# Kernel tuning notes

Measured on AMD Instinct MI355X. Metric: run time of the kernel, lower is better.

Reference implementation:

```python
import jax, jax.numpy as jnp
import numpy as np

K = 50
EPS = 1e-8


def setup_inputs() -> dict:
    key = jax.random.key(0)
    k1, k2 = jax.random.split(key)
    B, S, V = 2, 2048, 50257
    p = jax.random.uniform(k1, (B, S, V), dtype=jnp.float32)
    q = jax.random.uniform(k2, (B, S, V), dtype=jnp.float32)
    # normalize to probability distributions over the vocab dim
    p = p / jnp.sum(p, axis=-1, keepdims=True)
    q = q / jnp.sum(q, axis=-1, keepdims=True)
    return {"p": p, "q": q}


def _kl(p, q):
    p_safe = p + EPS
    q_safe = q + EPS
    return jnp.sum(p_safe * jnp.log(p_safe / q_safe), axis=-1)


def reference(p, q):
    B, S, V = p.shape
    N = B * S
    p_flat = p.reshape(N, V)
    q_flat = q.reshape(N, V)

    _, p_idx = jax.lax.top_k(p_flat, K)  # [N, K]
    _, q_idx = jax.lax.top_k(q_flat, K)  # [N, K]

    rows = jnp.arange(N)[:, None]  # [N, 1]
    mask = jnp.zeros((N, V), dtype=bool)
    mask = mask.at[rows, p_idx].set(True)
    mask = mask.at[rows, q_idx].set(True)

    p_m = jnp.where(mask, p_flat, 0.0)
    q_m = jnp.where(mask, q_flat, 0.0)

    p_m = p_m / (jnp.sum(p_m, axis=-1, keepdims=True) + EPS)
    q_m = q_m / (jnp.sum(q_m, axis=-1, keepdims=True) + EPS)

    m = 0.5 * (p_m + q_m)
    jsd = 0.5 * _kl(p_m, m) + 0.5 * _kl(q_m, m)  # [N]
    return jsd.reshape(B, S)
```

## Files before the change

### kernel.cpp

```cpp
#include <hip/hip_runtime.h>
#include <stdint.h>

#define NTHREADS 256
#define KTOP 50
#define CAP 1024
#define CAPREF 512
#define EPSV 1e-8f

typedef unsigned long long u64;

#define C_CNTP 0
#define C_CNTQ 1
#define C_REFP 2
#define C_REFQ 3

__device__ __forceinline__ float block_max(float v, float* s_f, int tid) {
    for (int off = 32; off; off >>= 1) v = fmaxf(v, __shfl_down(v, off));
    if ((tid & 63) == 0) s_f[tid >> 6] = v;
    __syncthreads();
    if (tid == 0) {
        float m = s_f[0];
        for (int w = 1; w < NTHREADS / 64; ++w) m = fmaxf(m, s_f[w]);
        s_f[4] = m;
    }
    __syncthreads();
    float r = s_f[4];
    __syncthreads();
    return r;
}

__device__ __forceinline__ void push_cand(u64* cand, uint32_t* cnt,
                                          float v, int idx, float t) {
    if (v >= t) {
        uint32_t pos = atomicAdd(cnt, 1u);
        if (pos < CAP)
            cand[pos] = (((u64)__float_as_uint(v)) << 16) |
                        (u64)(0xFFFFu - (uint32_t)idx);
    }
}

__device__ int collect_direct(const float* __restrict__ row, int V, float t,
                              u64* cand, uint32_t* s_cnt, int tid) {
    if (tid == 0) *s_cnt = 0;
    __syncthreads();
    int mis = (int)(((uintptr_t)row >> 2) & 3);
    int head = (4 - mis) & 3; if (head > V) head = V;
    if (tid < head) push_cand(cand, s_cnt, row[tid], tid, t);
    int nvec = (V - head) >> 2;
    const float4* vr = reinterpret_cast<const float4*>(row + head);
    for (int i = tid; i < nvec; i += NTHREADS) {
        float4 v = vr[i];
        int b = head + (i << 2);
        push_cand(cand, s_cnt, v.x, b, t);     push_cand(cand, s_cnt, v.y, b + 1, t);
        push_cand(cand, s_cnt, v.z, b + 2, t); push_cand(cand, s_cnt, v.w, b + 3, t);
    }
    for (int i = head + (nvec << 2) + tid; i < V; i += NTHREADS)
        push_cand(cand, s_cnt, row[i], i, t);
    __syncthreads();
    int n = (int)*s_cnt;
    __syncthreads();
    return n;
}

__device__ __forceinline__ float max16(float4 a, float4 b, float4 c, float4 d) {
    float m0 = fmaxf(fmaxf(a.x, a.y), fmaxf(a.z, a.w));
    float m1 = fmaxf(fmaxf(b.x, b.y), fmaxf(b.z, b.w));
    float m2 = fmaxf(fmaxf(c.x, c.y), fmaxf(c.z, c.w));
    float m3 = fmaxf(fmaxf(d.x, d.y), fmaxf(d.z, d.w));
    return fmaxf(fmaxf(m0, m1), fmaxf(m2, m3));
}

__device__ void find_topk(const u64* cand, int nc, uint16_t* top,
                          u64* s_merge, int tid) {
    int lane = tid & 63, w = tid >> 6;
    u64 r0 = 0, r1 = 0, r2 = 0, r3 = 0;
    int j0 = (w << 6) + lane;
    if (j0 < nc)       r0 = cand[j0];
    if (j0 + 256 < nc) r1 = cand[j0 + 256];
    if (j0 + 512 < nc) r2 = cand[j0 + 512];
    if (j0 + 768 < nc) r3 = cand[j0 + 768];
    for (int k = 0; k < KTOP; ++k) {
        u64 a = r0 > r1 ? r0 : r1;
        u64 b = r2 > r3 ? r2 : r3;
        u64 m = a > b ? a : b;
        #pragma unroll
        for (int off = 32; off; off >>= 1) {
            u64 o = __shfl_xor(m, off);
            if (o > m) m = o;
        }
        if (lane == 0) s_merge[w * KTOP + k] = m;
        if (r0 == m) r0 = 0; else if (r1 == m) r1 = 0;
        else if (r2 == m) r2 = 0; else if (r3 == m) r3 = 0;
    }
    __syncthreads();
    if (w == 0) {
        u64 q0 = 0, q1 = 0, q2 = 0, q3 = 0;
        if (lane < 4 * KTOP)       q0 = s_merge[lane];
        if (lane + 64 < 4 * KTOP)  q1 = s_merge[lane + 64];
        if (lane + 128 < 4 * KTOP) q2 = s_merge[lane + 128];
        if (lane + 192 < 4 * KTOP) q3 = s_merge[lane + 192];
        for (int k = 0; k < KTOP; ++k) {
            u64 a = q0 > q1 ? q0 : q1;
            u64 b = q2 > q3 ? q2 : q3;
            u64 m = a > b ? a : b;
            #pragma unroll
            for (int off = 32; off; off >>= 1) {
                u64 o = __shfl_xor(m, off);
                if (o > m) m = o;
            }
            if (lane == 0) top[k] = (uint16_t)(0xFFFFu - (uint32_t)(m & 0xFFFFu));
            if (q0 == m) q0 = 0; else if (q1 == m) q1 = 0;
            else if (q2 == m) q2 = 0; else if (q3 == m) q3 = 0;
        }
    }
    __syncthreads();
}

__global__ __launch_bounds__(NTHREADS, 4)
void topk_jsd_kernel(const float* __restrict__ p, const float* __restrict__ q,
                     float* __restrict__ out, int V)
{
    __shared__ u64 candP[CAP];
    __shared__ u64 candQ[CAP];
    __shared__ uint32_t refsP[CAPREF];
    __shared__ uint32_t refsQ[CAPREF];
    __shared__ u64 s_merge[4 * KTOP];
    __shared__ float s_f[8];
    __shared__ uint32_t s_c[4];
    __shared__ uint16_t topP[KTOP];
    __shared__ uint16_t topQ[KTOP];
    __shared__ uint16_t s_union[2 * KTOP];
    __shared__ int s_nu;

    const int row = blockIdx.x;
    const int tid = threadIdx.x;
    const float* prow = p + (size_t)row * (size_t)V;
    const float* qrow = q + (size_t)row * (size_t)V;

    int smp = V < 2048 ? V : 2048;
    float msP = 0.f, msQ = 0.f;
    for (int i = tid; i < smp; i += NTHREADS) {
        msP = fmaxf(msP, prow[i]);
        msQ = fmaxf(msQ, qrow[i]);
    }
    float MsP = block_max(msP, s_f, tid);
    float MsQ = block_max(msQ, s_f, tid);

    float eps0 = fminf(128.f / (float)V + 1.f / (float)smp, 0.5f);
    float tP = MsP * (1.f - eps0);
    float tQ = MsQ * (1.f - eps0);

    int misP = (int)(((uintptr_t)prow >> 2) & 3);
    int misQ = (int)(((uintptr_t)qrow >> 2) & 3);
    int headP = (4 - misP) & 3; if (headP > V) headP = V;
    int headQ = (4 - misQ) & 3; if (headQ > V) headQ = V;

    int ncP = -1, ncQ = -1;
    if (headP == headQ) {
        int head = headP;
        if (tid == 0) { s_c[0] = 0; s_c[1] = 0; s_c[2] = 0; s_c[3] = 0; }
        __syncthreads();
        int nvec = (V - head) >> 2;
        const float4* vp = reinterpret_cast<const float4*>(prow + head);
        const float4* vq = reinterpret_cast<const float4*>(qrow + head);
        const int per = 4 * NTHREADS;
        int ngrp = nvec / per;

        if (tid < head) {
            push_cand(candP, &s_c[C_CNTP], prow[tid], tid, tP);
            push_cand(candQ, &s_c[C_CNTQ], qrow[tid], tid, tQ);
        }
        #pragma unroll 2
        for (int g = 0; g < ngrp; ++g) {
            int o = g * per + tid;
            float4 a0 = vp[o];
            float4 a1 = vp[o + NTHREADS];
            float4 a2 = vp[o + 2 * NTHREADS];
            float4 a3 = vp[o + 3 * NTHREADS];
            float4 b0 = vq[o];
            float4 b1 = vq[o + NTHREADS];
            float4 b2 = vq[o + 2 * NTHREADS];
            float4 b3 = vq[o + 3 * NTHREADS];
            float mp = max16(a0, a1, a2, a3);
            float mq = max16(b0, b1, b2, b3);
            if (mp >= tP) {
                uint32_t rp = atomicAdd(&s_c[C_REFP], 1u);
                if (rp < CAPREF) refsP[rp] = (uint32_t)o;
            }
            if (mq >= tQ) {
                uint32_t rq = atomicAdd(&s_c[C_REFQ], 1u);
                if (rq < CAPREF) refsQ[rq] = (uint32_t)o;
            }
        }
        for (int i = ngrp * per + tid; i < nvec; i += NTHREADS) {
            float4 a = vp[i], b = vq[i];
            int e = head + (i << 2);
            push_cand(candP, &s_c[C_CNTP], a.x, e, tP);     push_cand(candP, &s_c[C_CNTP], a.y, e + 1, tP);
            push_cand(candP, &s_c[C_CNTP], a.z, e + 2, tP); push_cand(candP, &s_c[C_CNTP], a.w, e + 3, tP);
            push_cand(candQ, &s_c[C_CNTQ], b.x, e, tQ);     push_cand(candQ, &s_c[C_CNTQ], b.y, e + 1, tQ);
            push_cand(candQ, &s_c[C_CNTQ], b.z, e + 2, tQ); push_cand(candQ, &s_c[C_CNTQ], b.w, e + 3, tQ);
        }
        for (int i = head + (nvec << 2) + tid; i < V; i += NTHREADS) {
            push_cand(candP, &s_c[C_CNTP], prow[i], i, tP);
            push_cand(candQ, &s_c[C_CNTQ], qrow[i], i, tQ);
        }
        __syncthreads();
        uint32_t nrefP = s_c[C_REFP], nrefQ = s_c[C_REFQ];
        if (nrefP <= CAPREF) {
            int units = (int)nrefP * 4;
            for (int u = tid; u < units; u += NTHREADS) {
                int f4 = (int)refsP[u >> 2] + (u & 3) * NTHREADS;
                float4 v = vp[f4];
                int e = head + (f4 << 2);
                push_cand(candP, &s_c[C_CNTP], v.x, e, tP);     push_cand(candP, &s_c[C_CNTP], v.y, e + 1, tP);
                push_cand(candP, &s_c[C_CNTP], v.z, e + 2, tP); push_cand(candP, &s_c[C_CNTP], v.w, e + 3, tP);
            }
        }
        if (nrefQ <= CAPREF) {
            int units = (int)nrefQ * 4;
            for (int u = tid; u < units; u += NTHREADS) {
                int f4 = (int)refsQ[u >> 2] + (u & 3) * NTHREADS;
                float4 v = vq[f4];
                int e = head + (f4 << 2);
                push_cand(candQ, &s_c[C_CNTQ], v.x, e, tQ);     push_cand(candQ, &s_c[C_CNTQ], v.y, e + 1, tQ);
                push_cand(candQ, &s_c[C_CNTQ], v.z, e + 2, tQ); push_cand(candQ, &s_c[C_CNTQ], v.w, e + 3, tQ);
            }
        }
        __syncthreads();
        ncP = (nrefP <= CAPREF) ? (int)s_c[C_CNTP] : -1;
        ncQ = (nrefQ <= CAPREF) ? (int)s_c[C_CNTQ] : -1;
        __syncthreads();
    }

    {
        float eps = eps0;
        if (ncP < 0) ncP = collect_direct(prow, V, MsP * (1.f - eps), candP, &s_c[C_CNTP], tid);
        for (int a = 0; a < 10 && (ncP < KTOP || ncP > CAP); ++a) {
            eps = (ncP > CAP) ? eps * 0.25f : fminf(eps * 4.f, 1.f);
            ncP = collect_direct(prow, V, MsP * (1.f - eps), candP, &s_c[C_CNTP], tid);
        }
        if (ncP > CAP) ncP = CAP;
    }
    {
        float eps = eps0;
        if (ncQ < 0) ncQ = collect_direct(qrow, V, MsQ * (1.f - eps), candQ, &s_c[C_CNTQ], tid);
        for (int a = 0; a < 10 && (ncQ < KTOP || ncQ > CAP); ++a) {
            eps = (ncQ > CAP) ? eps * 0.25f : fminf(eps * 4.f, 1.f);
            ncQ = collect_direct(qrow, V, MsQ * (1.f - eps), candQ, &s_c[C_CNTQ], tid);
        }
        if (ncQ > CAP) ncQ = CAP;
    }

    find_topk(candP, ncP, topP, s_merge, tid);
    find_topk(candQ, ncQ, topQ, s_merge, tid);

    if (tid < KTOP) s_union[tid] = topP[tid];
    __syncthreads();
    if (tid < 64) {
        bool fresh = false; uint16_t qi = 0;
        if (tid < KTOP) {
            qi = topQ[tid]; fresh = true;
            for (int j = 0; j < KTOP; ++j) if (topP[j] == qi) fresh = false;
        }
        unsigned long long mb = __ballot(fresh);
        int pos = __popcll(mb & ((1ull << tid) - 1ull));
        if (fresh) s_union[KTOP + pos] = qi;
        if (tid == 0) s_nu = KTOP + __popcll(mb);
    }
    __syncthreads();
    int nu = s_nu;

    float pv = 0.f, qv = 0.f;
    if (tid < nu) {
        int ui = s_union[tid];
        pv = prow[ui];
        qv = qrow[ui];
    }

    float sp = pv, sq = qv;
    for (int off = 32; off; off >>= 1) { sp += __shfl_down(sp, off); sq += __shfl_down(sq, off); }
    int wid = tid >> 6;
    if ((tid & 63) == 0) { s_f[wid] = sp; s_f[4 + wid] = sq; }
    __syncthreads();
    if (tid == 0) {
        float a = 0.f, b = 0.f;
        for (int w = 0; w < NTHREADS / 64; ++w) { a += s_f[w]; b += s_f[4 + w]; }
        s_f[0] = a; s_f[4] = b;
    }
    __syncthreads();
    float sump = s_f[0], sumq = s_f[4];
    __syncthreads();

    float term = 0.f;
    if (tid < nu) {
        float pn = pv / (sump + EPSV);
        float qn = qv / (sumq + EPSV);
        float mn = 0.5f * (pn + qn);
        float ps = pn + EPSV, qs = qn + EPSV, ms = mn + EPSV;
        term = 0.5f * (ps * logf(ps / ms) + qs * logf(qs / ms));
    }
    for (int off = 32; off; off >>= 1) term += __shfl_down(term, off);
    if ((tid & 63) == 0) s_f[wid] = term;
    __syncthreads();
    if (tid == 0) {
        float a = 0.f;
        for (int w = 0; w < NTHREADS / 64; ++w) a += s_f[w];
        out[row] = a;
    }
}

extern "C" void kernel_launch(void* const* d_in, const int* in_sizes, int n_in,
                              void* d_out, int out_size, void* d_ws, size_t ws_size,
                              hipStream_t stream) {
    const float* p = (const float*)d_in[0];
    const float* q = (const float*)d_in[1];
    float* out = (float*)d_out;
    if (out_size <= 0) return;
    int N = out_size;
    int V = in_sizes[0] / N;
    topk_jsd_kernel<<<dim3(N), dim3(NTHREADS), 0, stream>>>(p, q, out, V);
}
```

Baseline: 476.4 us.

## Pipeline threshold scan with register masks and 32-bit candidates, parallel per-wave top-k

The main threshold scan is rewritten as a software-pipelined double-buffered loop with scheduling hints. Hit groups are recorded in per-thread bitmasks instead of shared-memory ref lists with atomics. Candidates are packed as 32-bit (value delta from threshold, index) keys to halve LDS use, and the top-50 selection for P and Q runs concurrently on separate single waves. Overflow of the 16-bit delta or a bad count falls back to the old 64-bit path, which adds complexity and a rescan when that happens.

```diff
diff --git a/kernel.cpp b/kernel.cpp
--- a/kernel.cpp
+++ b/kernel.cpp
@@ -4,15 +4,16 @@
 #define NTHREADS 256
 #define KTOP 50
 #define CAP 1024
-#define CAPREF 512
 #define EPSV 1e-8f
+#define MAXGRP 32
 
 typedef unsigned long long u64;
+typedef uint32_t u32;
 
 #define C_CNTP 0
 #define C_CNTQ 1
-#define C_REFP 2
-#define C_REFQ 3
+#define C_OVF  2
+#define C_GEN  3
 
 __device__ __forceinline__ float block_max(float v, float* s_f, int tid) {
     for (int off = 32; off; off >>= 1) v = fmaxf(v, __shfl_down(v, off));
@@ -29,49 +30,51 @@
     return r;
 }
 
-__device__ __forceinline__ void push_cand(u64* cand, uint32_t* cnt,
-                                          float v, int idx, float t) {
+__device__ __forceinline__ void push32(u32* cand, u32* cnt, u32* ovf,
+                                       float v, int idx, float t, u32 tbits) {
     if (v >= t) {
-        uint32_t pos = atomicAdd(cnt, 1u);
+        u32 delta = __float_as_uint(v) - tbits;
+        if (delta > 0xFFFFu) { *ovf = 1u; delta = 0xFFFFu; }
+        u32 pos = atomicAdd(cnt, 1u);
+        if (pos < CAP) cand[pos] = (delta << 16) | (0xFFFFu - (u32)idx);
+    }
+}
+
+__device__ __forceinline__ void push64(u64* cand, u32* cnt,
+                                       float v, int idx, float t) {
+    if (v >= t) {
+        u32 pos = atomicAdd(cnt, 1u);
         if (pos < CAP)
             cand[pos] = (((u64)__float_as_uint(v)) << 16) |
-                        (u64)(0xFFFFu - (uint32_t)idx);
-    }
-}
-
-__device__ int collect_direct(const float* __restrict__ row, int V, float t,
-                              u64* cand, uint32_t* s_cnt, int tid) {
+                        (u64)(0xFFFFu - (u32)idx);
+    }
+}
+
+__device__ int collect_direct64(const float* __restrict__ row, int V, float t,
+                                u64* cand, u32* s_cnt, int tid) {
     if (tid == 0) *s_cnt = 0;
     __syncthreads();
     int mis = (int)(((uintptr_t)row >> 2) & 3);
     int head = (4 - mis) & 3; if (head > V) head = V;
-    if (tid < head) push_cand(cand, s_cnt, row[tid], tid, t);
+    if (tid < head) push64(cand, s_cnt, row[tid], tid, t);
     int nvec = (V - head) >> 2;
     const float4* vr = reinterpret_cast<const float4*>(row + head);
     for (int i = tid; i < nvec; i += NTHREADS) {
         float4 v = vr[i];
         int b = head + (i << 2);
-        push_cand(cand, s_cnt, v.x, b, t);     push_cand(cand, s_cnt, v.y, b + 1, t);
-        push_cand(cand, s_cnt, v.z, b + 2, t); push_cand(cand, s_cnt, v.w, b + 3, t);
+        push64(cand, s_cnt, v.x, b, t);     push64(cand, s_cnt, v.y, b + 1, t);
+        push64(cand, s_cnt, v.z, b + 2, t); push64(cand, s_cnt, v.w, b + 3, t);
     }
     for (int i = head + (nvec << 2) + tid; i < V; i += NTHREADS)
-        push_cand(cand, s_cnt, row[i], i, t);
+        push64(cand, s_cnt, row[i], i, t);
     __syncthreads();
     int n = (int)*s_cnt;
     __syncthreads();
     return n;
 }
 
-__device__ __forceinline__ float max16(float4 a, float4 b, float4 c, float4 d) {
-    float m0 = fmaxf(fmaxf(a.x, a.y), fmaxf(a.z, a.w));
-    float m1 = fmaxf(fmaxf(b.x, b.y), fmaxf(b.z, b.w));
-    float m2 = fmaxf(fmaxf(c.x, c.y), fmaxf(c.z, c.w));
-    float m3 = fmaxf(fmaxf(d.x, d.y), fmaxf(d.z, d.w));
-    return fmaxf(fmaxf(m0, m1), fmaxf(m2, m3));
-}
-
-__device__ void find_topk(const u64* cand, int nc, uint16_t* top,
-                          u64* s_merge, int tid) {
+__device__ void find_topk64(const u64* cand, int nc, uint16_t* top,
+                            u64* s_merge, int tid) {
     int lane = tid & 63, w = tid >> 6;
     u64 r0 = 0, r1 = 0, r2 = 0, r3 = 0;
     int j0 = (w << 6) + lane;
@@ -108,32 +111,83 @@
                 u64 o = __shfl_xor(m, off);
                 if (o > m) m = o;
             }
-            if (lane == 0) top[k] = (uint16_t)(0xFFFFu - (uint32_t)(m & 0xFFFFu));
+            if (lane == 0) top[k] = (uint16_t)(0xFFFFu - (u32)(m & 0xFFFFu));
             if (q0 == m) q0 = 0; else if (q1 == m) q1 = 0;
             else if (q2 == m) q2 = 0; else if (q3 == m) q3 = 0;
         }
     }
     __syncthreads();
 }
+
+template <int NR>
+__device__ void find32(const u32* cand, int nc, uint16_t* top, int lane) {
+    u32 r[NR];
+    #pragma unroll
+    for (int j = 0; j < NR; ++j) {
+        int idx = lane + j * 64;
+        r[j] = (idx < nc) ? cand[idx] : 0u;
+    }
+    u32 mine = 0;
+    for (int k = 0; k < KTOP; ++k) {
+        u32 m = 0;
+        #pragma unroll
+        for (int j = 0; j < NR; ++j) m = r[j] > m ? r[j] : m;
+        #pragma unroll
+        for (int off = 32; off; off >>= 1) {
+            u32 o = __shfl_xor(m, off);
+            m = o > m ? o : m;
+        }
+        if (lane == k) mine = m;
+        #pragma unroll
+        for (int j = 0; j < NR; ++j) if (r[j] == m) r[j] = 0;
+    }
+    if (lane < KTOP) top[lane] = (uint16_t)(0xFFFFu - (mine & 0xFFFFu));
+}
+
+__device__ __forceinline__ float max16(float4 a, float4 b, float4 c, float4 d) {
+    float m0 = fmaxf(fmaxf(a.x, a.y), fmaxf(a.z, a.w));
+    float m1 = fmaxf(fmaxf(b.x, b.y), fmaxf(b.z, b.w));
+    float m2 = fmaxf(fmaxf(c.x, c.y), fmaxf(c.z, c.w));
+    float m3 = fmaxf(fmaxf(d.x, d.y), fmaxf(d.z, d.w));
+    return fmaxf(fmaxf(m0, m1), fmaxf(m2, m3));
+}
+
+#define PER4 (4 * NTHREADS)
+
+#define LOADG(P0,P1,P2,P3,Q0,Q1,Q2,Q3,g) do { int _o = (g) * PER4 + tid; \
+    P0 = vp[_o]; P1 = vp[_o + NTHREADS]; P2 = vp[_o + 2*NTHREADS]; P3 = vp[_o + 3*NTHREADS]; \
+    Q0 = vq[_o]; Q1 = vq[_o + NTHREADS]; Q2 = vq[_o + 2*NTHREADS]; Q3 = vq[_o + 3*NTHREADS]; } while (0)
+
+#define CONSUME(P0,P1,P2,P3,Q0,Q1,Q2,Q3,g) do { \
+    float _mp = max16(P0,P1,P2,P3); float _mq = max16(Q0,Q1,Q2,Q3); \
+    maskP |= (_mp >= tP) ? (1u << (g)) : 0u; \
+    maskQ |= (_mq >= tQ) ? (1u << (g)) : 0u; } while (0)
+
+#define SCHED_HINT() do { \
+    __builtin_amdgcn_sched_group_barrier(0x020, 8, 0); \
+    __builtin_amdgcn_sched_group_barrier(0x002, 60, 0); \
+    __builtin_amdgcn_sched_group_barrier(0x020, 8, 0); \
+    __builtin_amdgcn_sched_group_barrier(0x002, 60, 0); } while (0)
 
 __global__ __launch_bounds__(NTHREADS, 4)
 void topk_jsd_kernel(const float* __restrict__ p, const float* __restrict__ q,
                      float* __restrict__ out, int V)
 {
-    __shared__ u64 candP[CAP];
-    __shared__ u64 candQ[CAP];
-    __shared__ uint32_t refsP[CAPREF];
-    __shared__ uint32_t refsQ[CAPREF];
+    __shared__ u64 candRaw[CAP];
     __shared__ u64 s_merge[4 * KTOP];
     __shared__ float s_f[8];
-    __shared__ uint32_t s_c[4];
+    __shared__ u32 s_c[4];
     __shared__ uint16_t topP[KTOP];
     __shared__ uint16_t topQ[KTOP];
     __shared__ uint16_t s_union[2 * KTOP];
     __shared__ int s_nu;
 
+    u32* candP = (u32*)candRaw;
+    u32* candQ = ((u32*)candRaw) + CAP;
+
     const int row = blockIdx.x;
     const int tid = threadIdx.x;
+    const int lane = tid & 63, w = tid >> 6;
     const float* prow = p + (size_t)row * (size_t)V;
     const float* qrow = q + (size_t)row * (size_t)V;
 
@@ -149,122 +203,146 @@
     float eps0 = fminf(128.f / (float)V + 1.f / (float)smp, 0.5f);
     float tP = MsP * (1.f - eps0);
     float tQ = MsQ * (1.f - eps0);
+    u32 tPb = __float_as_uint(tP), tQb = __float_as_uint(tQ);
 
     int misP = (int)(((uintptr_t)prow >> 2) & 3);
     int misQ = (int)(((uintptr_t)qrow >> 2) & 3);
     int headP = (4 - misP) & 3; if (headP > V) headP = V;
     int headQ = (4 - misQ) & 3; if (headQ > V) headQ = V;
+    bool fast = (headP == headQ);
 
     int ncP = -1, ncQ = -1;
-    if (headP == headQ) {
+    u32 ovf = 1;
+
+    if (fast) {
         int head = headP;
-        if (tid == 0) { s_c[0] = 0; s_c[1] = 0; s_c[2] = 0; s_c[3] = 0; }
+        if (tid == 0) { s_c[0] = 0; s_c[1] = 0; s_c[2] = 0; }
         __syncthreads();
         int nvec = (V - head) >> 2;
         const float4* vp = reinterpret_cast<const float4*>(prow + head);
         const float4* vq = reinterpret_cast<const float4*>(qrow + head);
-        const int per = 4 * NTHREADS;
-        int ngrp = nvec / per;
+        int ngrp_full = nvec / PER4;
+        int ngrp = ngrp_full < MAXGRP ? ngrp_full : MAXGRP;
+
+        u32 maskP = 0, maskQ = 0;
+        float4 pa0, pa1, pa2, pa3, qa0, qa1, qa2, qa3;
+        float4 pb0, pb1, pb2, pb3, qb0, qb1, qb2, qb3;
+
+        int g = 0;
+        if (ngrp > 0) LOADG(pa0,pa1,pa2,pa3,qa0,qa1,qa2,qa3, 0);
+        for (; g + 2 < ngrp; g += 2) {
+            LOADG(pb0,pb1,pb2,pb3,qb0,qb1,qb2,qb3, g + 1);
+            CONSUME(pa0,pa1,pa2,pa3,qa0,qa1,qa2,qa3, g);
+            LOADG(pa0,pa1,pa2,pa3,qa0,qa1,qa2,qa3, g + 2);
+            CONSUME(pb0,pb1,pb2,pb3,qb0,qb1,qb2,qb3, g + 1);
+            SCHED_HINT();
+        }
+        if (ngrp - g == 2) {
+            LOADG(pb0,pb1,pb2,pb3,qb0,qb1,qb2,qb3, g + 1);
+            CONSUME(pa0,pa1,pa2,pa3,qa0,qa1,qa2,qa3, g);
+            CONSUME(pb0,pb1,pb2,pb3,qb0,qb1,qb2,qb3, g + 1);
+        } else if (ngrp - g == 1) {
+            CONSUME(pa0,pa1,pa2,pa3,qa0,qa1,qa2,qa3, g);
+        }
 
         if (tid < head) {
-            push_cand(candP, &s_c[C_CNTP], prow[tid], tid, tP);
-            push_cand(candQ, &s_c[C_CNTQ], qrow[tid], tid, tQ);
-        }
-        #pragma unroll 2
-        for (int g = 0; g < ngrp; ++g) {
-            int o = g * per + tid;
-            float4 a0 = vp[o];
-            float4 a1 = vp[o + NTHREADS];
-            float4 a2 = vp[o + 2 * NTHREADS];
-            float4 a3 = vp[o + 3 * NTHREADS];
-            float4 b0 = vq[o];
-            float4 b1 = vq[o + NTHREADS];
-            float4 b2 = vq[o + 2 * NTHREADS];
-            float4 b3 = vq[o + 3 * NTHREADS];
-            float mp = max16(a0, a1, a2, a3);
-            float mq = max16(b0, b1, b2, b3);
-            if (mp >= tP) {
-                uint32_t rp = atomicAdd(&s_c[C_REFP], 1u);
-                if (rp < CAPREF) refsP[rp] = (uint32_t)o;
-            }
-            if (mq >= tQ) {
-                uint32_t rq = atomicAdd(&s_c[C_REFQ], 1u);
-                if (rq < CAPREF) refsQ[rq] = (uint32_t)o;
-            }
-        }
-        for (int i = ngrp * per + tid; i < nvec; i += NTHREADS) {
+            push32(candP, &s_c[C_CNTP], &s_c[C_OVF], prow[tid], tid, tP, tPb);
+            push32(candQ, &s_c[C_CNTQ], &s_c[C_OVF], qrow[tid], tid, tQ, tQb);
+        }
+        for (int i = ngrp * PER4 + tid; i < nvec; i += NTHREADS) {
             float4 a = vp[i], b = vq[i];
             int e = head + (i << 2);
-            push_cand(candP, &s_c[C_CNTP], a.x, e, tP);     push_cand(candP, &s_c[C_CNTP], a.y, e + 1, tP);
-            push_cand(candP, &s_c[C_CNTP], a.z, e + 2, tP); push_cand(candP, &s_c[C_CNTP], a.w, e + 3, tP);
-            push_cand(candQ, &s_c[C_CNTQ], b.x, e, tQ);     push_cand(candQ, &s_c[C_CNTQ], b.y, e + 1, tQ);
-            push_cand(candQ, &s_c[C_CNTQ], b.z, e + 2, tQ); push_cand(candQ, &s_c[C_CNTQ], b.w, e + 3, tQ);
+            push32(candP, &s_c[C_CNTP], &s_c[C_OVF], a.x, e,     tP, tPb);
+            push32(candP, &s_c[C_CNTP], &s_c[C_OVF], a.y, e + 1, tP, tPb);
+            push32(candP, &s_c[C_CNTP], &s_c[C_OVF], a.z, e + 2, tP, tPb);
+            push32(candP, &s_c[C_CNTP], &s_c[C_OVF], a.w, e + 3, tP, tPb);
+            push32(candQ, &s_c[C_CNTQ], &s_c[C_OVF], b.x, e,     tQ, tQb);
+            push32(candQ, &s_c[C_CNTQ], &s_c[C_OVF], b.y, e + 1, tQ, tQb);
+            push32(candQ, &s_c[C_CNTQ], &s_c[C_OVF], b.z, e + 2, tQ, tQb);
+            push32(candQ, &s_c[C_CNTQ], &s_c[C_OVF], b.w, e + 3, tQ, tQb);
         }
         for (int i = head + (nvec << 2) + tid; i < V; i += NTHREADS) {
-            push_cand(candP, &s_c[C_CNTP], prow[i], i, tP);
-            push_cand(candQ, &s_c[C_CNTQ], qrow[i], i, tQ);
+            push32(candP, &s_c[C_CNTP], &s_c[C_OVF], prow[i], i, tP, tPb);
+            push32(candQ, &s_c[C_CNTQ], &s_c[C_OVF], qrow[i], i, tQ, tQb);
+        }
+        while (maskP) {
+            int gb = __ffs(maskP) - 1; maskP &= maskP - 1;
+            int o = gb * PER4 + tid;
+            #pragma unroll
+            for (int j = 0; j < 4; ++j) {
+                float4 v = vp[o + j * NTHREADS];
+                int e = head + ((o + j * NTHREADS) << 2);
+                push32(candP, &s_c[C_CNTP], &s_c[C_OVF], v.x, e,     tP, tPb);
+                push32(candP, &s_c[C_CNTP], &s_c[C_OVF], v.y, e + 1, tP, tPb);
+                push32(candP, &s_c[C_CNTP], &s_c[C_OVF], v.z, e + 2, tP, tPb);
+                push32(candP, &s_c[C_CNTP], &s_c[C_OVF], v.w, e + 3, tP, tPb);
+            }
+        }
+        while (maskQ) {
+            int gb = __ffs(maskQ) - 1; maskQ &= maskQ - 1;
+            int o = gb * PER4 + tid;
+            #pragma unroll
+            for (int j = 0; j < 4; ++j) {
+                float4 v = vq[o + j * NTHREADS];
+                int e = head + ((o + j * NTHREADS) << 2);
+                push32(candQ, &s_c[C_CNTQ], &s_c[C_OVF], v.x, e,     tQ, tQb);
+                push32(candQ, &s_c[C_CNTQ], &s_c[C_OVF], v.y, e + 1, tQ, tQb);
+                push32(candQ, &s_c[C_CNTQ], &s_c[C_OVF], v.z, e + 2, tQ, tQb);
+                push32(candQ, &s_c[C_CNTQ], &s_c[C_OVF], v.w, e + 3, tQ, tQb);
+            }
         }
         __syncthreads();
-        uint32_t nrefP = s_c[C_REFP], nrefQ = s_c[C_REFQ];
-        if (nrefP <= CAPREF) {
-            int units = (int)nrefP * 4;
-            for (int u = tid; u < units; u += NTHREADS) {
-                int f4 = (int)refsP[u >> 2] + (u & 3) * NTHREADS;
-                float4 v = vp[f4];
-                int e = head + (f4 << 2);
-                push_cand(candP, &s_c[C_CNTP], v.x, e, tP);     push_cand(candP, &s_c[C_CNTP], v.y, e + 1, tP);
-                push_cand(candP, &s_c[C_CNTP], v.z, e + 2, tP); push_cand(candP, &s_c[C_CNTP], v.w, e + 3, tP);
-            }
-        }
-        if (nrefQ <= CAPREF) {
-            int units = (int)nrefQ * 4;
-            for (int u = tid; u < units; u += NTHREADS) {
-                int f4 = (int)refsQ[u >> 2] + (u & 3) * NTHREADS;
-                float4 v = vq[f4];
-                int e = head + (f4 << 2);
-                push_cand(candQ, &s_c[C_CNTQ], v.x, e, tQ);     push_cand(candQ, &s_c[C_CNTQ], v.y, e + 1, tQ);
-                push_cand(candQ, &s_c[C_CNTQ], v.z, e + 2, tQ); push_cand(candQ, &s_c[C_CNTQ], v.w, e + 3, tQ);
-            }
-        }
+        ncP = (int)s_c[C_CNTP];
+        ncQ = (int)s_c[C_CNTQ];
+        ovf = s_c[C_OVF];
         __syncthreads();
-        ncP = (nrefP <= CAPREF) ? (int)s_c[C_CNTP] : -1;
-        ncQ = (nrefQ <= CAPREF) ? (int)s_c[C_CNTQ] : -1;
-        __syncthreads();
-    }
-
-    {
+    }
+
+    bool okP = fast && !ovf && ncP >= KTOP && ncP <= CAP;
+    bool okQ = fast && !ovf && ncQ >= KTOP && ncQ <= CAP;
+
+    if (okP && w == 0) {
+        if (ncP <= 256) find32<4>(candP, ncP, topP, lane);
+        else            find32<16>(candP, ncP, topP, lane);
+    }
+    if (okQ && w == 1) {
+        if (ncQ <= 256) find32<4>(candQ, ncQ, topQ, lane);
+        else            find32<16>(candQ, ncQ, topQ, lane);
+    }
+
+    if (!okP) {
         float eps = eps0;
-        if (ncP < 0) ncP = collect_direct(prow, V, MsP * (1.f - eps), candP, &s_c[C_CNTP], tid);
-        for (int a = 0; a < 10 && (ncP < KTOP || ncP > CAP); ++a) {
-            eps = (ncP > CAP) ? eps * 0.25f : fminf(eps * 4.f, 1.f);
-            ncP = collect_direct(prow, V, MsP * (1.f - eps), candP, &s_c[C_CNTP], tid);
-        }
-        if (ncP > CAP) ncP = CAP;
-    }
-    {
+        int nc = collect_direct64(prow, V, MsP * (1.f - eps), candRaw, &s_c[C_GEN], tid);
+        for (int a = 0; a < 10 && (nc < KTOP || nc > CAP); ++a) {
+            eps = (nc > CAP) ? eps * 0.25f : fminf(eps * 4.f, 1.f);
+            nc = collect_direct64(prow, V, MsP * (1.f - eps), candRaw, &s_c[C_GEN], tid);
+        }
+        if (nc > CAP) nc = CAP;
+        find_topk64(candRaw, nc, topP, s_merge, tid);
+    }
+    if (!okQ) {
         float eps = eps0;
-        if (ncQ < 0) ncQ = collect_direct(qrow, V, MsQ * (1.f - eps), candQ, &s_c[C_CNTQ], tid);
-        for (int a = 0; a < 10 && (ncQ < KTOP || ncQ > CAP); ++a) {
-            eps = (ncQ > CAP) ? eps * 0.25f : fminf(eps * 4.f, 1.f);
-            ncQ = collect_direct(qrow, V, MsQ * (1.f - eps), candQ, &s_c[C_CNTQ], tid);
-        }
-        if (ncQ > CAP) ncQ = CAP;
-    }
-
-    find_topk(candP, ncP, topP, s_merge, tid);
-    find_topk(candQ, ncQ, topQ, s_merge, tid);
+        int nc = collect_direct64(qrow, V, MsQ * (1.f - eps), candRaw, &s_c[C_GEN], tid);
+        for (int a = 0; a < 10 && (nc < KTOP || nc > CAP); ++a) {
+            eps = (nc > CAP) ? eps * 0.25f : fminf(eps * 4.f, 1.f);
+            nc = collect_direct64(qrow, V, MsQ * (1.f - eps), candRaw, &s_c[C_GEN], tid);
+        }
+        if (nc > CAP) nc = CAP;
+        find_topk64(candRaw, nc, topQ, s_merge, tid);
+    }
+    __syncthreads();
 
     if (tid < KTOP) s_union[tid] = topP[tid];
     __syncthreads();
     if (tid < 64) {
-        bool fresh = false; uint16_t qi = 0;
+        bool freshb = false; uint16_t qi = 0;
         if (tid < KTOP) {
-            qi = topQ[tid]; fresh = true;
-            for (int j = 0; j < KTOP; ++j) if (topP[j] == qi) fresh = false;
-        }
-        unsigned long long mb = __ballot(fresh);
+            qi = topQ[tid]; freshb = true;
+            for (int j = 0; j < KTOP; ++j) if (topP[j] == qi) freshb = false;
+        }
+        u64 mb = __ballot(freshb);
         int pos = __popcll(mb & ((1ull << tid) - 1ull));
-        if (fresh) s_union[KTOP + pos] = qi;
+        if (freshb) s_union[KTOP + pos] = qi;
         if (tid == 0) s_nu = KTOP + __popcll(mb);
     }
     __syncthreads();
@@ -272,19 +350,18 @@
 
     float pv = 0.f, qv = 0.f;
     if (tid < nu) {
-        int ui = s_union[tid];
+        int ui = s_union[tid]; ui = ui < V ? ui : V - 1;
         pv = prow[ui];
         qv = qrow[ui];
     }
 
     float sp = pv, sq = qv;
     for (int off = 32; off; off >>= 1) { sp += __shfl_down(sp, off); sq += __shfl_down(sq, off); }
-    int wid = tid >> 6;
-    if ((tid & 63) == 0) { s_f[wid] = sp; s_f[4 + wid] = sq; }
+    if ((tid & 63) == 0) { s_f[w] = sp; s_f[4 + w] = sq; }
     __syncthreads();
     if (tid == 0) {
         float a = 0.f, b = 0.f;
-        for (int w = 0; w < NTHREADS / 64; ++w) { a += s_f[w]; b += s_f[4 + w]; }
+        for (int ww = 0; ww < NTHREADS / 64; ++ww) { a += s_f[ww]; b += s_f[4 + ww]; }
         s_f[0] = a; s_f[4] = b;
     }
     __syncthreads();
@@ -300,11 +377,11 @@
         term = 0.5f * (ps * logf(ps / ms) + qs * logf(qs / ms));
     }
     for (int off = 32; off; off >>= 1) term += __shfl_down(term, off);
-    if ((tid & 63) == 0) s_f[wid] = term;
+    if ((tid & 63) == 0) s_f[w] = term;
     __syncthreads();
     if (tid == 0) {
         float a = 0.f;
-        for (int w = 0; w < NTHREADS / 64; ++w) a += s_f[w];
+        for (int ww = 0; ww < NTHREADS / 64; ++ww) a += s_f[ww];
         out[row] = a;
     }
 }
```

Result: slower. 492.3 us (+3.4%).
